# Kernel optimization log

Hardware: AMD Instinct MI355X
Metric: run time of the kernel (lower is better)

Reference implementation:

```python
import jax, jax.numpy as jnp
import numpy as np

N_HEADS = 16
HEAD_DIM = 64


def apply_rope(x, cos, sin):
    # x: [B, H, S, D]; cos/sin: [S, D//2]
    x_even = x[..., ::2]
    x_odd = x[..., 1::2]
    c = cos[None, None, :, :]
    s = sin[None, None, :, :]
    rot_even = x_even * c - x_odd * s
    rot_odd = x_even * s + x_odd * c
    return jnp.stack((rot_even, rot_odd), axis=-1).reshape(x.shape)


def setup_inputs() -> dict:
    key = jax.random.key(0)
    ks = jax.random.split(key, 7)
    B, S, D = 2, 2048, 1024
    x = jax.random.normal(ks[0], (B, S, D), dtype=jnp.float32)
    # realistic rope tables
    inv_freq = 1.0 / (10000.0 ** (np.arange(0, HEAD_DIM, 2, dtype=np.float32) / HEAD_DIM))
    t = np.arange(S, dtype=np.float32)
    freqs = np.outer(t, inv_freq)  # [S, HEAD_DIM//2]
    rope_cos = jnp.asarray(np.cos(freqs), dtype=jnp.float32)
    rope_sin = jnp.asarray(np.sin(freqs), dtype=jnp.float32)
    Wqkv = jax.random.normal(ks[1], (D, 3 * D), dtype=jnp.float32) * (D ** -0.5)
    bqkv = jax.random.normal(ks[2], (3 * D,), dtype=jnp.float32) * 0.02
    Wout = jax.random.normal(ks[3], (D, D), dtype=jnp.float32) * (D ** -0.5)
    bout = jax.random.normal(ks[4], (D,), dtype=jnp.float32) * 0.02
    return {"x": x, "rope_cos": rope_cos, "rope_sin": rope_sin,
            "Wqkv": Wqkv, "bqkv": bqkv, "Wout": Wout, "bout": bout}


def reference(x, rope_cos, rope_sin, Wqkv, bqkv, Wout, bout):
    B, S, D = x.shape
    H, Hd = N_HEADS, HEAD_DIM
    qkv = x @ Wqkv + bqkv                      # [B, S, 3D]
    qkv = qkv.reshape(B, S, 3, H, Hd).transpose(2, 0, 3, 1, 4)  # [3, B, H, S, Hd]
    q, k, v = qkv[0], qkv[1], qkv[2]
    q = apply_rope(q, rope_cos, rope_sin)
    k = apply_rope(k, rope_cos, rope_sin)
    scale = Hd ** -0.5
    scores = jnp.einsum('bhqd,bhkd->bhqk', q, k) * scale
    causal = jnp.tril(jnp.ones((S, S), dtype=bool))
    scores = jnp.where(causal[None, None], scores, jnp.finfo(scores.dtype).min)
    attn = jax.nn.softmax(scores, axis=-1)
    out = jnp.einsum('bhqk,bhkd->bhqd', attn, v)  # [B, H, S, Hd]
    out = out.transpose(0, 2, 1, 3).reshape(B, S, D)
    return out @ Wout + bout
```

## Files before the change

kernel.cpp:

```cpp
#include <hip/hip_runtime.h>
#include <hip/hip_bf16.h>

typedef unsigned short u16;
typedef __attribute__((ext_vector_type(4))) float f32x4;
typedef __attribute__((ext_vector_type(16))) float f32x16;
typedef __attribute__((ext_vector_type(8))) short short8;
typedef __attribute__((ext_vector_type(8))) unsigned short ushort8;

__device__ __forceinline__ u16 f2bf(float f) {
  union { float f; unsigned u; } v; v.f = f;
  unsigned r = v.u + 0x7fffu + ((v.u >> 16) & 1u);
  return (u16)(r >> 16);
}
__device__ __forceinline__ float b2f(u16 h) {
  union { unsigned u; float f; } v; v.u = ((unsigned)h) << 16;
  return v.f;
}
__device__ __forceinline__ f32x4 mfma16(short8 a, short8 b, f32x4 c) {
  return __builtin_amdgcn_mfma_f32_16x16x32_bf16(a, b, c, 0, 0, 0);
}
__device__ __forceinline__ f32x16 mfma32(short8 a, short8 b, f32x16 c) {
  return __builtin_amdgcn_mfma_f32_32x32x16_bf16(a, b, c, 0, 0, 0);
}
__device__ __forceinline__ unsigned cvtpk(float a, float b) {
  unsigned r;
  asm("v_cvt_pk_bf16_f32 %0, %1, %2" : "=v"(r) : "v"(a), "v"(b));
  return r;
}
__device__ __forceinline__ short8 pack4(unsigned w0, unsigned w1, unsigned w2, unsigned w3) {
  union { unsigned u[4]; short8 s; } t;
  t.u[0] = w0; t.u[1] = w1; t.u[2] = w2; t.u[3] = w3;
  return t.s;
}
__device__ __forceinline__ float exp2h(float x) { return __builtin_amdgcn_exp2f(x); }

__global__ __launch_bounds__(256) void cvt_f32_bf16_k(const float* __restrict__ in,
                                                      u16* __restrict__ out, int n8) {
  int t = blockIdx.x * 256 + threadIdx.x;
  if (t >= n8) return;
  const float4* p = (const float4*)(in + (size_t)t * 8);
  float4 a = p[0], b = p[1];
  ushort8 o;
  o[0] = f2bf(a.x); o[1] = f2bf(a.y); o[2] = f2bf(a.z); o[3] = f2bf(a.w);
  o[4] = f2bf(b.x); o[5] = f2bf(b.y); o[6] = f2bf(b.z); o[7] = f2bf(b.w);
  *(ushort8*)(out + (size_t)t * 8) = o;
}

__global__ __launch_bounds__(256) void transpose_f32_bf16_k(const float* __restrict__ in,
                                                            u16* __restrict__ out, int R, int C) {
  __shared__ float tile[32][33];
  int bc = blockIdx.x * 32, br = blockIdx.y * 32;
  int tx = threadIdx.x & 31, ty = threadIdx.x >> 5;
#pragma unroll
  for (int p = 0; p < 4; ++p)
    tile[ty + p * 8][tx] = in[(size_t)(br + ty + p * 8) * C + bc + tx];
  __syncthreads();
#pragma unroll
  for (int p = 0; p < 4; ++p)
    out[(size_t)(bc + ty + p * 8) * R + br + tx] = f2bf(tile[tx][ty + p * 8]);
}

template <int MODE>
__global__ __launch_bounds__(256) void gemm_bt_k(const u16* __restrict__ A,
                                                 const u16* __restrict__ Bt,
                                                 const float* __restrict__ bias,
                                                 void* __restrict__ Cout) {
  __shared__ __align__(16) u16 As[128 * 32];
  __shared__ __align__(16) u16 Bs[128 * 32];
  const int tid = threadIdx.x, lane = tid & 63, w = tid >> 6;
  const int wr = w >> 1, wc = w & 1, g = lane >> 4, c16 = lane & 15;
  const int rowBase = blockIdx.y * 128, colBase = blockIdx.x * 128;
  f32x4 acc[4][4] = {};
  const int e0 = (w * 2 + 0) * 512 + lane * 8;
  const int e1 = (w * 2 + 1) * 512 + lane * 8;
  const u16* Ag0 = A + (size_t)(rowBase + (e0 >> 5)) * 1024 + (e0 & 31);
  const u16* Ag1 = A + (size_t)(rowBase + (e1 >> 5)) * 1024 + (e1 & 31);
  const u16* Bg0 = Bt + (size_t)(colBase + (e0 >> 5)) * 1024 + (e0 & 31);
  const u16* Bg1 = Bt + (size_t)(colBase + (e1 >> 5)) * 1024 + (e1 & 31);
  u16* As0 = As + (w * 2 + 0) * 512;
  u16* As1 = As + (w * 2 + 1) * 512;
  u16* Bs0 = Bs + (w * 2 + 0) * 512;
  u16* Bs1 = Bs + (w * 2 + 1) * 512;
  for (int k0 = 0; k0 < 1024; k0 += 32) {
    __builtin_amdgcn_global_load_lds((const __attribute__((address_space(1))) void*)(Ag0 + k0),
                                     (__attribute__((address_space(3))) void*)As0, 16, 0, 0);
    __builtin_amdgcn_global_load_lds((const __attribute__((address_space(1))) void*)(Ag1 + k0),
                                     (__attribute__((address_space(3))) void*)As1, 16, 0, 0);
    __builtin_amdgcn_global_load_lds((const __attribute__((address_space(1))) void*)(Bg0 + k0),
                                     (__attribute__((address_space(3))) void*)Bs0, 16, 0, 0);
    __builtin_amdgcn_global_load_lds((const __attribute__((address_space(1))) void*)(Bg1 + k0),
                                     (__attribute__((address_space(3))) void*)Bs1, 16, 0, 0);
    asm volatile("s_waitcnt vmcnt(0)" ::: "memory");
    __syncthreads();
    short8 af[4], bfr[4];
#pragma unroll
    for (int t = 0; t < 4; ++t)
      af[t] = *(const short8*)(As + ((wr * 64 + t * 16 + c16) * 32 + g * 8));
#pragma unroll
    for (int t = 0; t < 4; ++t)
      bfr[t] = *(const short8*)(Bs + ((wc * 64 + t * 16 + c16) * 32 + g * 8));
#pragma unroll
    for (int i = 0; i < 4; ++i)
#pragma unroll
      for (int j = 0; j < 4; ++j) acc[i][j] = mfma16(af[i], bfr[j], acc[i][j]);
    __syncthreads();
  }
#pragma unroll
  for (int i = 0; i < 4; ++i) {
    int mbase = rowBase + wr * 64 + i * 16 + 4 * g;
#pragma unroll
    for (int j = 0; j < 4; ++j) {
      int n = colBase + wc * 64 + j * 16 + c16;
      float bv = bias[n];
#pragma unroll
      for (int r = 0; r < 4; ++r) {
        float v = acc[i][j][r] + bv;
        int m = mbase + r;
        if (MODE == 0) {
          int which = n >> 10, hh = (n >> 6) & 15, d = n & 63;
          int bb = m >> 11, s = m & 2047;
          ((u16*)Cout)[((size_t)(((which * 2 + bb) * 16 + hh) * 2048 + s) << 6) + d] = f2bf(v);
        } else {
          ((float*)Cout)[(size_t)m * 1024 + n] = v;
        }
      }
    }
  }
}

__global__ __launch_bounds__(256) void rope_k(u16* __restrict__ qk, const float* __restrict__ cosT,
                                              const float* __restrict__ sinT, int npairs) {
  int p = blockIdx.x * 256 + threadIdx.x;
  if (p >= npairs) return;
  size_t E = (size_t)p * 2;
  int i = (int)((E >> 1) & 31);
  int s = (int)((E >> 6) & 2047);
  const float qs = (p < 2097152) ? 0.18033688f : 1.0f;
  u16* ptr = qk + E;
  float xe = b2f(ptr[0]), xo = b2f(ptr[1]);
  float c = cosT[s * 32 + i], sn = sinT[s * 32 + i];
  ptr[0] = f2bf((xe * c - xo * sn) * qs);
  ptr[1] = f2bf((xe * sn + xo * c) * qs);
}

__global__ __launch_bounds__(256) void vtrans_k(const u16* __restrict__ V, u16* __restrict__ Vt) {
  __shared__ u16 t[64][72];
  const int bh = blockIdx.y, s0 = blockIdx.x * 64;
  const u16* src = V + ((size_t)bh << 17);
  u16* dst = Vt + ((size_t)bh << 17);
  const int r = threadIdx.x >> 2, c0 = (threadIdx.x & 3) * 16;
  *(short8*)&t[r][c0] = *(const short8*)(src + (size_t)(s0 + r) * 64 + c0);
  *(short8*)&t[r][c0 + 8] = *(const short8*)(src + (size_t)(s0 + r) * 64 + c0 + 8);
  __syncthreads();
  const int d = threadIdx.x >> 2, sc0 = (threadIdx.x & 3) * 16;
  ushort8 o0, o1;
#pragma unroll
  for (int e = 0; e < 8; ++e) { o0[e] = t[sc0 + e][d]; o1[e] = t[sc0 + 8 + e][d]; }
  *(ushort8*)(dst + (size_t)d * 2048 + s0 + sc0) = o0;
  *(ushort8*)(dst + (size_t)d * 2048 + s0 + sc0 + 8) = o1;
}

__global__ __launch_bounds__(128, 4) void attn5_k(const u16* __restrict__ Qm,
                                                  const u16* __restrict__ Km,
                                                  const u16* __restrict__ Vtm,
                                                  u16* __restrict__ Om) {
  __shared__ __align__(16) u16 Klds[2][4096];
  __shared__ __align__(16) u16 Vlds[2][4096];

  const int lane = threadIdx.x & 63;
  const int w = threadIdx.x >> 6;
  const int x = blockIdx.x & 7;
  const int idx = blockIdx.x >> 3;
  const int bh = 4 * x + (idx & 3);
  const int qmb = 31 - (idx >> 2);
  const int b = bh >> 4, hd = bh & 15;
  const int qb = qmb * 64 + w * 32;
  const int q32 = lane & 31, h = lane >> 5;
  const int nt = qmb + 1;

  const u16* Qp = Qm + ((size_t)bh << 17);
  const u16* Kp = Km + ((size_t)bh << 17);
  const u16* Vtp = Vtm + ((size_t)bh << 17);

  const u16* qrow = Qp + ((size_t)(qb + q32) << 6) + 8 * h;
  short8 qf[4];
#pragma unroll
  for (int ks = 0; ks < 4; ++ks) qf[ks] = *(const short8*)(qrow + 16 * ks);

  f32x16 acc0 = {}, acc1 = {};
  float m_run = -1e30f, l_run = 0.f;
  const int qg = qb + q32;
  const int r8 = lane >> 3, blk = lane & 7;
  const int swz = q32 & 7;

  auto stage = [&](int buf, int k0) {
#pragma unroll
    for (int i = 0; i < 8; ++i) {
      const int row = i * 8 + r8;
      const int sblk = blk ^ (row & 7);
      if (w == 0) {
        const u16* src = Kp + ((size_t)(k0 + row) << 6) + sblk * 8;
        __builtin_amdgcn_global_load_lds(
            (const __attribute__((address_space(1))) void*)src,
            (__attribute__((address_space(3))) void*)(&Klds[buf][i * 512]), 16, 0, 0);
      } else {
        const u16* src = Vtp + ((size_t)row << 11) + k0 + sblk * 8;
        __builtin_amdgcn_global_load_lds(
            (const __attribute__((address_space(1))) void*)src,
            (__attribute__((address_space(3))) void*)(&Vlds[buf][i * 512]), 16, 0, 0);
      }
    }
  };

  stage(0, 0);
  asm volatile("s_waitcnt vmcnt(0)" ::: "memory");
  __syncthreads();

  for (int kt = 0; kt < nt; ++kt) {
    const int cur = kt & 1;
    if (kt + 1 < nt) stage(cur ^ 1, (kt + 1) * 64);

    const u16* Kb = &Klds[cur][0];
    const u16* Vb = &Vlds[cur][0];
    const int k0 = kt * 64;

    f32x16 s0 = {}, s1 = {};
    __builtin_amdgcn_s_setprio(1);
#pragma unroll
    for (int ks = 0; ks < 4; ++ks) {
      const int cb = ((2 * ks + h) ^ swz) * 8;
      short8 kf0 = *(const short8*)(Kb + q32 * 64 + cb);
      short8 kf1 = *(const short8*)(Kb + (32 + q32) * 64 + cb);
      s0 = mfma32(kf0, qf[ks], s0);
      s1 = mfma32(kf1, qf[ks], s1);
    }
    __builtin_amdgcn_s_setprio(0);

    short8 vfa[4], vfb[4];
#pragma unroll
    for (int ks = 0; ks < 4; ++ks) {
      const int cb = ((2 * ks + h) ^ swz) * 8;
      vfa[ks] = *(const short8*)(Vb + q32 * 64 + cb);
      vfb[ks] = *(const short8*)(Vb + (32 + q32) * 64 + cb);
    }

    if (kt == nt - 1) {
#pragma unroll
      for (int r = 0; r < 16; ++r) {
        const int kvl = k0 + (r & 3) + 8 * (r >> 2) + 4 * h;
        s0[r] = (kvl <= qg) ? s0[r] : -1e30f;
        s1[r] = (kvl + 32 <= qg) ? s1[r] : -1e30f;
      }
    }

    float pmax = s0[0];
#pragma unroll
    for (int r = 1; r < 16; ++r) pmax = fmaxf(pmax, s0[r]);
#pragma unroll
    for (int r = 0; r < 16; ++r) pmax = fmaxf(pmax, s1[r]);
    pmax = fmaxf(pmax, __shfl_xor(pmax, 32));

    if (!__all(pmax <= m_run + 11.5f)) {
      const float mn = fmaxf(m_run, pmax);
      const float alpha = exp2h(m_run - mn);
      l_run *= alpha;
      m_run = mn;
#pragma unroll
      for (int r = 0; r < 16; ++r) {
        const int row = (r & 3) + 8 * (r >> 2) + 4 * h;
        const float ar = __shfl(alpha, row);
        acc0[r] *= ar; acc1[r] *= ar;
      }
    }

    float rs = 0.f;
#pragma unroll
    for (int r = 0; r < 16; ++r) { s0[r] = exp2h(s0[r] - m_run); rs += s0[r]; }
#pragma unroll
    for (int r = 0; r < 16; ++r) { s1[r] = exp2h(s1[r] - m_run); rs += s1[r]; }
    rs += __shfl_xor(rs, 32);
    l_run += rs;

    short8 pa[4];
#pragma unroll
    for (int t = 0; t < 2; ++t) {
      float p0, p1, p2, p3, p4, p5, p6, p7, p8, p9, pa_, pb_, pc_, pd_, pe_, pf_;
      if (t == 0) {
        p0 = s0[0];  p1 = s0[1];  p2 = s0[2];  p3 = s0[3];
        p4 = s0[4];  p5 = s0[5];  p6 = s0[6];  p7 = s0[7];
        p8 = s0[8];  p9 = s0[9];  pa_ = s0[10]; pb_ = s0[11];
        pc_ = s0[12]; pd_ = s0[13]; pe_ = s0[14]; pf_ = s0[15];
      } else {
        p0 = s1[0];  p1 = s1[1];  p2 = s1[2];  p3 = s1[3];
        p4 = s1[4];  p5 = s1[5];  p6 = s1[6];  p7 = s1[7];
        p8 = s1[8];  p9 = s1[9];  pa_ = s1[10]; pb_ = s1[11];
        pc_ = s1[12]; pd_ = s1[13]; pe_ = s1[14]; pf_ = s1[15];
      }
      const unsigned a0 = cvtpk(p0, p1), a1 = cvtpk(p2, p3);
      const unsigned a2 = cvtpk(p4, p5), a3 = cvtpk(p6, p7);
      const unsigned b0 = cvtpk(p8, p9), b1 = cvtpk(pa_, pb_);
      const unsigned b2 = cvtpk(pc_, pd_), b3 = cvtpk(pe_, pf_);
      const unsigned r0 = __shfl_xor(h ? a0 : a2, 32);
      const unsigned r1 = __shfl_xor(h ? a1 : a3, 32);
      pa[2 * t] = h ? pack4(r0, r1, a2, a3) : pack4(a0, a1, r0, r1);
      const unsigned r2 = __shfl_xor(h ? b0 : b2, 32);
      const unsigned r3 = __shfl_xor(h ? b1 : b3, 32);
      pa[2 * t + 1] = h ? pack4(r2, r3, b2, b3) : pack4(b0, b1, r2, r3);
    }

    __builtin_amdgcn_s_setprio(1);
#pragma unroll
    for (int ks = 0; ks < 4; ++ks) {
      acc0 = mfma32(pa[ks], vfa[ks], acc0);
      acc1 = mfma32(pa[ks], vfb[ks], acc1);
    }
    __builtin_amdgcn_s_setprio(0);

    asm volatile("s_waitcnt vmcnt(0)" ::: "memory");
    __syncthreads();
  }

#pragma unroll
  for (int r = 0; r < 16; ++r) {
    const int row = (r & 3) + 8 * (r >> 2) + 4 * h;
    const float li = 1.0f / __shfl(l_run, row);
    const int q = qb + row;
    const size_t base = ((size_t)(b * 2048 + q) << 10) + hd * 64 + q32;
    Om[base] = f2bf(acc0[r] * li);
    Om[base + 32] = f2bf(acc1[r] * li);
  }
}

extern "C" void kernel_launch(void* const* d_in, const int* in_sizes, int n_in,
                              void* d_out, int out_size, void* d_ws, size_t ws_size,
                              hipStream_t stream) {
  const float* x        = (const float*)d_in[0];
  const float* rope_cos = (const float*)d_in[1];
  const float* rope_sin = (const float*)d_in[2];
  const float* Wqkv     = (const float*)d_in[3];
  const float* bqkv     = (const float*)d_in[4];
  const float* Wout     = (const float*)d_in[5];
  const float* bout     = (const float*)d_in[6];
  float* out = (float*)d_out;
  char* ws = (char*)d_ws;

  u16* Xb      = (u16*)(ws);
  u16* WqkvT   = (u16*)(ws + 8388608);
  u16* WoutT   = (u16*)(ws + 14680064);
  u16* QKV     = (u16*)(ws + 16777216);
  u16* AttnOut = (u16*)(ws + 41943040);
  u16* Vt      = (u16*)(ws + 50331648);

  cvt_f32_bf16_k<<<dim3(2048), dim3(256), 0, stream>>>(x, Xb, 524288);
  transpose_f32_bf16_k<<<dim3(96, 32), dim3(256), 0, stream>>>(Wqkv, WqkvT, 1024, 3072);
  transpose_f32_bf16_k<<<dim3(32, 32), dim3(256), 0, stream>>>(Wout, WoutT, 1024, 1024);

  gemm_bt_k<0><<<dim3(24, 32), dim3(256), 0, stream>>>(Xb, WqkvT, bqkv, (void*)QKV);

  rope_k<<<dim3(16384), dim3(256), 0, stream>>>(QKV, rope_cos, rope_sin, 4194304);

  u16* Qw = QKV;
  u16* Kw = QKV + (size_t)4194304;
  u16* Vw = QKV + (size_t)8388608;
  vtrans_k<<<dim3(32, 32), dim3(256), 0, stream>>>(Vw, Vt);
  attn5_k<<<dim3(1024), dim3(128), 0, stream>>>(Qw, Kw, Vt, AttnOut);

  gemm_bt_k<1><<<dim3(8, 32), dim3(256), 0, stream>>>(AttnOut, WoutT, bout, out);
}
```

Measured before the change: 151.9 us.

## Fuse RoPE into QKV GEMM epilogue and split attention KV range across wave halves

Removes the separate RoPE kernel by applying the rotation and the Q scale in the QKV GEMM epilogue. It uses a lane shuffle to fetch the even/odd partner, which is valid because adjacent columns sit in adjacent lanes. The attention kernel now uses 512-thread blocks covering 128 query rows. Two groups of four waves each process half of the KV tiles, and their partial softmax states are merged through LDS at the end. This is meant to cut the serial KV loop length per wave and drop a memory pass, at the cost of merge overhead and some idle iterations on masked tiles.

```diff
diff --git a/kernel.cpp b/kernel.cpp
--- a/kernel.cpp
+++ b/kernel.cpp
@@ -64,6 +64,8 @@
 __global__ __launch_bounds__(256) void gemm_bt_k(const u16* __restrict__ A,
                                                  const u16* __restrict__ Bt,
                                                  const float* __restrict__ bias,
+                                                 const float* __restrict__ cosT,
+                                                 const float* __restrict__ sinT,
                                                  void* __restrict__ Cout) {
   __shared__ __align__(16) u16 As[128 * 32];
   __shared__ __align__(16) u16 Bs[128 * 32];
@@ -119,28 +121,21 @@
         if (MODE == 0) {
           int which = n >> 10, hh = (n >> 6) & 15, d = n & 63;
           int bb = m >> 11, s = m & 2047;
-          ((u16*)Cout)[((size_t)(((which * 2 + bb) * 16 + hh) * 2048 + s) << 6) + d] = f2bf(v);
+          float outv = v;
+          if (which < 2) {
+            float pv = __shfl_xor(v, 1);
+            float cc = cosT[(size_t)s * 32 + (d >> 1)];
+            float ss = sinT[(size_t)s * 32 + (d >> 1)];
+            outv = (d & 1) ? (v * cc + pv * ss) : (v * cc - pv * ss);
+            if (which == 0) outv *= 0.18033688f;
+          }
+          ((u16*)Cout)[((size_t)(((which * 2 + bb) * 16 + hh) * 2048 + s) << 6) + d] = f2bf(outv);
         } else {
           ((float*)Cout)[(size_t)m * 1024 + n] = v;
         }
       }
     }
   }
-}
-
-__global__ __launch_bounds__(256) void rope_k(u16* __restrict__ qk, const float* __restrict__ cosT,
-                                              const float* __restrict__ sinT, int npairs) {
-  int p = blockIdx.x * 256 + threadIdx.x;
-  if (p >= npairs) return;
-  size_t E = (size_t)p * 2;
-  int i = (int)((E >> 1) & 31);
-  int s = (int)((E >> 6) & 2047);
-  const float qs = (p < 2097152) ? 0.18033688f : 1.0f;
-  u16* ptr = qk + E;
-  float xe = b2f(ptr[0]), xo = b2f(ptr[1]);
-  float c = cosT[s * 32 + i], sn = sinT[s * 32 + i];
-  ptr[0] = f2bf((xe * c - xo * sn) * qs);
-  ptr[1] = f2bf((xe * sn + xo * c) * qs);
 }
 
 __global__ __launch_bounds__(256) void vtrans_k(const u16* __restrict__ V, u16* __restrict__ Vt) {
@@ -160,29 +155,32 @@
   *(ushort8*)(dst + (size_t)d * 2048 + s0 + sc0 + 8) = o1;
 }
 
-__global__ __launch_bounds__(128, 4) void attn5_k(const u16* __restrict__ Qm,
+__global__ __launch_bounds__(512, 4) void attn6_k(const u16* __restrict__ Qm,
                                                   const u16* __restrict__ Km,
                                                   const u16* __restrict__ Vtm,
                                                   u16* __restrict__ Om) {
-  __shared__ __align__(16) u16 Klds[2][4096];
-  __shared__ __align__(16) u16 Vlds[2][4096];
-
-  const int lane = threadIdx.x & 63;
-  const int w = threadIdx.x >> 6;
+  __shared__ __align__(16) u16 smem[32768];
+  u16* KL = smem;
+  u16* VL = smem + 16384;
+
+  const int tid = threadIdx.x;
+  const int lane = tid & 63, w = tid >> 6;
+  const int usub = w & 3, half = w >> 2;
   const int x = blockIdx.x & 7;
   const int idx = blockIdx.x >> 3;
   const int bh = 4 * x + (idx & 3);
-  const int qmb = 31 - (idx >> 2);
+  const int qmb = 15 - (idx >> 2);
   const int b = bh >> 4, hd = bh & 15;
-  const int qb = qmb * 64 + w * 32;
-  const int q32 = lane & 31, h = lane >> 5;
-  const int nt = qmb + 1;
+  const int qb = qmb * 128 + usub * 32;
+  const int q32 = lane & 31, hl = lane >> 5;
+  const int NTH = qmb + 1;
+  const int tbase = half * NTH;
 
   const u16* Qp = Qm + ((size_t)bh << 17);
   const u16* Kp = Km + ((size_t)bh << 17);
   const u16* Vtp = Vtm + ((size_t)bh << 17);
 
-  const u16* qrow = Qp + ((size_t)(qb + q32) << 6) + 8 * h;
+  const u16* qrow = Qp + ((size_t)(qb + q32) << 6) + 8 * hl;
   short8 qf[4];
 #pragma unroll
   for (int ks = 0; ks < 4; ++ks) qf[ks] = *(const short8*)(qrow + 16 * ks);
@@ -193,141 +191,167 @@
   const int r8 = lane >> 3, blk = lane & 7;
   const int swz = q32 & 7;
 
-  auto stage = [&](int buf, int k0) {
-#pragma unroll
-    for (int i = 0; i < 8; ++i) {
-      const int row = i * 8 + r8;
-      const int sblk = blk ^ (row & 7);
-      if (w == 0) {
-        const u16* src = Kp + ((size_t)(k0 + row) << 6) + sblk * 8;
-        __builtin_amdgcn_global_load_lds(
-            (const __attribute__((address_space(1))) void*)src,
-            (__attribute__((address_space(3))) void*)(&Klds[buf][i * 512]), 16, 0, 0);
-      } else {
-        const u16* src = Vtp + ((size_t)row << 11) + k0 + sblk * 8;
-        __builtin_amdgcn_global_load_lds(
-            (const __attribute__((address_space(1))) void*)src,
-            (__attribute__((address_space(3))) void*)(&Vlds[buf][i * 512]), 16, 0, 0);
-      }
+  auto stage = [&](int buf, int k0s) {
+#pragma unroll
+    for (int t = 0; t < 2; ++t) {
+      const int c = usub * 2 + t;
+      const int row = c * 8 + r8;
+      const int sblk = blk ^ r8;
+      const u16* ksrc = Kp + ((size_t)(k0s + row) << 6) + sblk * 8;
+      __builtin_amdgcn_global_load_lds(
+          (const __attribute__((address_space(1))) void*)ksrc,
+          (__attribute__((address_space(3))) void*)(KL + (half * 2 + buf) * 4096 + c * 512),
+          16, 0, 0);
+      const u16* vsrc = Vtp + ((size_t)row << 11) + k0s + sblk * 8;
+      __builtin_amdgcn_global_load_lds(
+          (const __attribute__((address_space(1))) void*)vsrc,
+          (__attribute__((address_space(3))) void*)(VL + (half * 2 + buf) * 4096 + c * 512),
+          16, 0, 0);
     }
   };
 
-  stage(0, 0);
+  stage(0, 64 * tbase);
   asm volatile("s_waitcnt vmcnt(0)" ::: "memory");
   __syncthreads();
 
-  for (int kt = 0; kt < nt; ++kt) {
-    const int cur = kt & 1;
-    if (kt + 1 < nt) stage(cur ^ 1, (kt + 1) * 64);
-
-    const u16* Kb = &Klds[cur][0];
-    const u16* Vb = &Vlds[cur][0];
-    const int k0 = kt * 64;
-
-    f32x16 s0 = {}, s1 = {};
-    __builtin_amdgcn_s_setprio(1);
-#pragma unroll
-    for (int ks = 0; ks < 4; ++ks) {
-      const int cb = ((2 * ks + h) ^ swz) * 8;
-      short8 kf0 = *(const short8*)(Kb + q32 * 64 + cb);
-      short8 kf1 = *(const short8*)(Kb + (32 + q32) * 64 + cb);
-      s0 = mfma32(kf0, qf[ks], s0);
-      s1 = mfma32(kf1, qf[ks], s1);
-    }
-    __builtin_amdgcn_s_setprio(0);
-
-    short8 vfa[4], vfb[4];
-#pragma unroll
-    for (int ks = 0; ks < 4; ++ks) {
-      const int cb = ((2 * ks + h) ^ swz) * 8;
-      vfa[ks] = *(const short8*)(Vb + q32 * 64 + cb);
-      vfb[ks] = *(const short8*)(Vb + (32 + q32) * 64 + cb);
-    }
-
-    if (kt == nt - 1) {
-#pragma unroll
-      for (int r = 0; r < 16; ++r) {
-        const int kvl = k0 + (r & 3) + 8 * (r >> 2) + 4 * h;
-        s0[r] = (kvl <= qg) ? s0[r] : -1e30f;
-        s1[r] = (kvl + 32 <= qg) ? s1[r] : -1e30f;
-      }
-    }
-
-    float pmax = s0[0];
-#pragma unroll
-    for (int r = 1; r < 16; ++r) pmax = fmaxf(pmax, s0[r]);
-#pragma unroll
-    for (int r = 0; r < 16; ++r) pmax = fmaxf(pmax, s1[r]);
-    pmax = fmaxf(pmax, __shfl_xor(pmax, 32));
-
-    if (!__all(pmax <= m_run + 11.5f)) {
-      const float mn = fmaxf(m_run, pmax);
-      const float alpha = exp2h(m_run - mn);
-      l_run *= alpha;
-      m_run = mn;
-#pragma unroll
-      for (int r = 0; r < 16; ++r) {
-        const int row = (r & 3) + 8 * (r >> 2) + 4 * h;
-        const float ar = __shfl(alpha, row);
-        acc0[r] *= ar; acc1[r] *= ar;
-      }
-    }
-
-    float rs = 0.f;
-#pragma unroll
-    for (int r = 0; r < 16; ++r) { s0[r] = exp2h(s0[r] - m_run); rs += s0[r]; }
-#pragma unroll
-    for (int r = 0; r < 16; ++r) { s1[r] = exp2h(s1[r] - m_run); rs += s1[r]; }
-    rs += __shfl_xor(rs, 32);
-    l_run += rs;
-
-    short8 pa[4];
-#pragma unroll
-    for (int t = 0; t < 2; ++t) {
-      float p0, p1, p2, p3, p4, p5, p6, p7, p8, p9, pa_, pb_, pc_, pd_, pe_, pf_;
-      if (t == 0) {
-        p0 = s0[0];  p1 = s0[1];  p2 = s0[2];  p3 = s0[3];
-        p4 = s0[4];  p5 = s0[5];  p6 = s0[6];  p7 = s0[7];
-        p8 = s0[8];  p9 = s0[9];  pa_ = s0[10]; pb_ = s0[11];
-        pc_ = s0[12]; pd_ = s0[13]; pe_ = s0[14]; pf_ = s0[15];
-      } else {
-        p0 = s1[0];  p1 = s1[1];  p2 = s1[2];  p3 = s1[3];
-        p4 = s1[4];  p5 = s1[5];  p6 = s1[6];  p7 = s1[7];
-        p8 = s1[8];  p9 = s1[9];  pa_ = s1[10]; pb_ = s1[11];
-        pc_ = s1[12]; pd_ = s1[13]; pe_ = s1[14]; pf_ = s1[15];
-      }
-      const unsigned a0 = cvtpk(p0, p1), a1 = cvtpk(p2, p3);
-      const unsigned a2 = cvtpk(p4, p5), a3 = cvtpk(p6, p7);
-      const unsigned b0 = cvtpk(p8, p9), b1 = cvtpk(pa_, pb_);
-      const unsigned b2 = cvtpk(pc_, pd_), b3 = cvtpk(pe_, pf_);
-      const unsigned r0 = __shfl_xor(h ? a0 : a2, 32);
-      const unsigned r1 = __shfl_xor(h ? a1 : a3, 32);
-      pa[2 * t] = h ? pack4(r0, r1, a2, a3) : pack4(a0, a1, r0, r1);
-      const unsigned r2 = __shfl_xor(h ? b0 : b2, 32);
-      const unsigned r3 = __shfl_xor(h ? b1 : b3, 32);
-      pa[2 * t + 1] = h ? pack4(r2, r3, b2, b3) : pack4(b0, b1, r2, r3);
-    }
-
-    __builtin_amdgcn_s_setprio(1);
-#pragma unroll
-    for (int ks = 0; ks < 4; ++ks) {
-      acc0 = mfma32(pa[ks], vfa[ks], acc0);
-      acc1 = mfma32(pa[ks], vfb[ks], acc1);
-    }
-    __builtin_amdgcn_s_setprio(0);
+  for (int i = 0; i < NTH; ++i) {
+    const int cur = i & 1;
+    if (i + 1 < NTH) stage(cur ^ 1, 64 * (tbase + i + 1));
+    const int k0 = 64 * (tbase + i);
+
+    if (k0 <= qb + 31) {
+      const u16* Kb = KL + (half * 2 + cur) * 4096;
+      const u16* Vb = VL + (half * 2 + cur) * 4096;
+
+      f32x16 s0 = {}, s1 = {};
+      __builtin_amdgcn_s_setprio(1);
+#pragma unroll
+      for (int ks = 0; ks < 4; ++ks) {
+        const int cb = ((2 * ks + hl) ^ swz) * 8;
+        short8 kf0 = *(const short8*)(Kb + q32 * 64 + cb);
+        short8 kf1 = *(const short8*)(Kb + (32 + q32) * 64 + cb);
+        s0 = mfma32(kf0, qf[ks], s0);
+        s1 = mfma32(kf1, qf[ks], s1);
+      }
+      __builtin_amdgcn_s_setprio(0);
+
+      short8 vfa[4], vfb[4];
+#pragma unroll
+      for (int ks = 0; ks < 4; ++ks) {
+        const int cb = ((2 * ks + hl) ^ swz) * 8;
+        vfa[ks] = *(const short8*)(Vb + q32 * 64 + cb);
+        vfb[ks] = *(const short8*)(Vb + (32 + q32) * 64 + cb);
+      }
+
+      if (k0 + 63 > qb) {
+#pragma unroll
+        for (int r = 0; r < 16; ++r) {
+          const int kvl = k0 + (r & 3) + 8 * (r >> 2) + 4 * hl;
+          s0[r] = (kvl <= qg) ? s0[r] : -1e30f;
+          s1[r] = (kvl + 32 <= qg) ? s1[r] : -1e30f;
+        }
+      }
+
+      float pmax = s0[0];
+#pragma unroll
+      for (int r = 1; r < 16; ++r) pmax = fmaxf(pmax, s0[r]);
+#pragma unroll
+      for (int r = 0; r < 16; ++r) pmax = fmaxf(pmax, s1[r]);
+      pmax = fmaxf(pmax, __shfl_xor(pmax, 32));
+
+      if (!__all(pmax <= m_run + 11.5f)) {
+        const float mn = fmaxf(m_run, pmax);
+        const float alpha = exp2h(m_run - mn);
+        l_run *= alpha;
+        m_run = mn;
+#pragma unroll
+        for (int r = 0; r < 16; ++r) {
+          const int row = (r & 3) + 8 * (r >> 2) + 4 * hl;
+          const float ar = __shfl(alpha, row);
+          acc0[r] *= ar; acc1[r] *= ar;
+        }
+      }
+
+      float rs = 0.f;
+#pragma unroll
+      for (int r = 0; r < 16; ++r) { s0[r] = exp2h(s0[r] - m_run); rs += s0[r]; }
+#pragma unroll
+      for (int r = 0; r < 16; ++r) { s1[r] = exp2h(s1[r] - m_run); rs += s1[r]; }
+      rs += __shfl_xor(rs, 32);
+      l_run += rs;
+
+      short8 pa[4];
+#pragma unroll
+      for (int t = 0; t < 2; ++t) {
+        float p0, p1, p2, p3, p4, p5, p6, p7, p8, p9, pa_, pb_, pc_, pd_, pe_, pf_;
+        if (t == 0) {
+          p0 = s0[0];  p1 = s0[1];  p2 = s0[2];  p3 = s0[3];
+          p4 = s0[4];  p5 = s0[5];  p6 = s0[6];  p7 = s0[7];
+          p8 = s0[8];  p9 = s0[9];  pa_ = s0[10]; pb_ = s0[11];
+          pc_ = s0[12]; pd_ = s0[13]; pe_ = s0[14]; pf_ = s0[15];
+        } else {
+          p0 = s1[0];  p1 = s1[1];  p2 = s1[2];  p3 = s1[3];
+          p4 = s1[4];  p5 = s1[5];  p6 = s1[6];  p7 = s1[7];
+          p8 = s1[8];  p9 = s1[9];  pa_ = s1[10]; pb_ = s1[11];
+          pc_ = s1[12]; pd_ = s1[13]; pe_ = s1[14]; pf_ = s1[15];
+        }
+        const unsigned a0 = cvtpk(p0, p1), a1 = cvtpk(p2, p3);
+        const unsigned a2 = cvtpk(p4, p5), a3 = cvtpk(p6, p7);
+        const unsigned b0 = cvtpk(p8, p9), b1 = cvtpk(pa_, pb_);
+        const unsigned b2 = cvtpk(pc_, pd_), b3 = cvtpk(pe_, pf_);
+        const unsigned r0 = __shfl_xor(hl ? a0 : a2, 32);
+        const unsigned r1 = __shfl_xor(hl ? a1 : a3, 32);
+        pa[2 * t] = hl ? pack4(r0, r1, a2, a3) : pack4(a0, a1, r0, r1);
+        const unsigned r2 = __shfl_xor(hl ? b0 : b2, 32);
+        const unsigned r3 = __shfl_xor(hl ? b1 : b3, 32);
+        pa[2 * t + 1] = hl ? pack4(r2, r3, b2, b3) : pack4(b0, b1, r2, r3);
+      }
+
+      __builtin_amdgcn_s_setprio(1);
+#pragma unroll
+      for (int ks = 0; ks < 4; ++ks) {
+        acc0 = mfma32(pa[ks], vfa[ks], acc0);
+        acc1 = mfma32(pa[ks], vfb[ks], acc1);
+      }
+      __builtin_amdgcn_s_setprio(0);
+    }
 
     asm volatile("s_waitcnt vmcnt(0)" ::: "memory");
     __syncthreads();
   }
 
-#pragma unroll
-  for (int r = 0; r < 16; ++r) {
-    const int row = (r & 3) + 8 * (r >> 2) + 4 * h;
-    const float li = 1.0f / __shfl(l_run, row);
-    const int q = qb + row;
-    const size_t base = ((size_t)(b * 2048 + q) << 10) + hd * 64 + q32;
-    Om[base] = f2bf(acc0[r] * li);
-    Om[base + 32] = f2bf(acc1[r] * li);
+  float* mbuf = (float*)(void*)smem;
+  float* mu = mbuf + usub * (34 * 64);
+  if (half == 1) {
+    mu[lane] = m_run;
+    mu[64 + lane] = l_run;
+#pragma unroll
+    for (int r = 0; r < 16; ++r) {
+      mu[(2 + r) * 64 + lane] = acc0[r];
+      mu[(18 + r) * 64 + lane] = acc1[r];
+    }
+  }
+  __syncthreads();
+  if (half == 0) {
+    const float m_o = mu[lane];
+    const float l_o = mu[64 + lane];
+    const float M = fmaxf(m_run, m_o);
+    const float ss = exp2h(m_run - M);
+    const float so = exp2h(m_o - M);
+    const float l_c = l_run * ss + l_o * so;
+#pragma unroll
+    for (int r = 0; r < 16; ++r) {
+      const int row = (r & 3) + 8 * (r >> 2) + 4 * hl;
+      const float ssr = __shfl(ss, row);
+      const float sor = __shfl(so, row);
+      const float li = 1.0f / __shfl(l_c, row);
+      const float o0 = (acc0[r] * ssr + mu[(2 + r) * 64 + lane] * sor) * li;
+      const float o1 = (acc1[r] * ssr + mu[(18 + r) * 64 + lane] * sor) * li;
+      const int q = qb + row;
+      const size_t base = ((size_t)(b * 2048 + q) << 10) + hd * 64 + q32;
+      Om[base] = f2bf(o0);
+      Om[base + 32] = f2bf(o1);
+    }
   }
 }
 
@@ -355,15 +379,14 @@
   transpose_f32_bf16_k<<<dim3(96, 32), dim3(256), 0, stream>>>(Wqkv, WqkvT, 1024, 3072);
   transpose_f32_bf16_k<<<dim3(32, 32), dim3(256), 0, stream>>>(Wout, WoutT, 1024, 1024);
 
-  gemm_bt_k<0><<<dim3(24, 32), dim3(256), 0, stream>>>(Xb, WqkvT, bqkv, (void*)QKV);
-
-  rope_k<<<dim3(16384), dim3(256), 0, stream>>>(QKV, rope_cos, rope_sin, 4194304);
+  gemm_bt_k<0><<<dim3(24, 32), dim3(256), 0, stream>>>(Xb, WqkvT, bqkv, rope_cos, rope_sin,
+                                                       (void*)QKV);
 
   u16* Qw = QKV;
   u16* Kw = QKV + (size_t)4194304;
   u16* Vw = QKV + (size_t)8388608;
   vtrans_k<<<dim3(32, 32), dim3(256), 0, stream>>>(Vw, Vt);
-  attn5_k<<<dim3(1024), dim3(128), 0, stream>>>(Qw, Kw, Vt, AttnOut);
-
-  gemm_bt_k<1><<<dim3(8, 32), dim3(256), 0, stream>>>(AttnOut, WoutT, bout, out);
-}
+  attn6_k<<<dim3(512), dim3(512), 0, stream>>>(Qw, Kw, Vt, AttnOut);
+
+  gemm_bt_k<1><<<dim3(8, 32), dim3(256), 0, stream>>>(AttnOut, WoutT, bout, nullptr, nullptr, out);
+}
```

Result: slower. 155.9 us (+2.6%).
